# Kernel optimization log

Hardware: AMD Instinct MI355X
Metric: run time of the kernel (lower is better)

The kernel has to match this reference:

```python
import jax, jax.numpy as jnp
import numpy as np

# Hough voting constants from the call site:
# Hough(angle=90, R2_list=[4,64,256,1024], num_classes=1, region_num=13, vote_field_size=33)
ANGLE = 90
R2_LIST = (4, 64, 256, 1024)
REGION_NUM = 13
VFS = 33  # vote field size


def _hough_filter():
    """Log-polar vote-field filter [region_num, VFS, VFS].

    Region 0 = center disk (r^2 <= R2_LIST[0]); region 1 + ring*4 + angle_bin
    for the 3 radius rings x 4 angle sectors. Each region's weights are
    1/(#pixels in region) so each region's vote sums to 1 (HoughNet log map).
    """
    c = VFS // 2
    ys, xs = np.meshgrid(np.arange(VFS) - c, np.arange(VFS) - c, indexing='ij')
    r2 = xs ** 2 + ys ** 2
    theta = (np.degrees(np.arctan2(ys, xs)) + 360.0) % 360.0
    nang = 360 // ANGLE  # 4 angle sectors
    abin = np.minimum((theta // ANGLE).astype(np.int64), nang - 1)
    region = -np.ones((VFS, VFS), np.int64)
    region[r2 <= R2_LIST[0]] = 0
    for i in range(1, len(R2_LIST)):
        m = (r2 > R2_LIST[i - 1]) & (r2 <= R2_LIST[i])
        region[m] = 1 + (i - 1) * nang + abin[m]
    filt = np.zeros((REGION_NUM, VFS, VFS), np.float32)
    for r in range(REGION_NUM):
        m = region == r
        if m.sum() > 0:
            filt[r][m] = 1.0 / float(m.sum())
    return filt


# ConvTranspose2d(13 -> 1, k=33, stride=1, pad=16) == SAME conv with flipped kernel.
_HOUGH_CONV_W = jnp.asarray(np.flip(_hough_filter(), axis=(1, 2))[None].copy())  # [1,13,33,33]


def setup_inputs() -> dict:
    key = jax.random.key(0)
    ks = jax.random.split(key, 4)
    B, C, H, W = 2, 256, 256, 512
    return {
        'x': jax.random.normal(ks[0], (B, C, H, W), jnp.float32),
        'pos_w': jax.random.normal(ks[1], (13, C), jnp.float32) * 0.05,
        'pos_b': jnp.zeros((13,), jnp.float32),
        'reg_w': jax.random.normal(ks[2], (1, C), jnp.float32) * 0.05,
        'reg_b': jnp.zeros((1,), jnp.float32),
        'off_w': jax.random.normal(ks[3], (2, C), jnp.float32) * 0.05,
        'off_b': jnp.zeros((2,), jnp.float32),
    }


def _conv1x1(x, w, b):
    # x: [B,C,H,W], w: [O,C] -> [B,O,H,W]
    return jnp.einsum('bchw,oc->bohw', x, w) + b[None, :, None, None]


def reference(x, pos_w, pos_b, reg_w, reg_b, off_w, off_b):
    evident = jax.nn.relu(_conv1x1(x, pos_w, pos_b))  # [B,13,H,W]
    score = jax.lax.conv_general_dilated(
        evident, _HOUGH_CONV_W, (1, 1), 'SAME',
        dimension_numbers=('NCHW', 'OIHW', 'NCHW'))  # [B,1,H,W]
    x_cls = jax.nn.sigmoid(score)
    x_reg = _conv1x1(x, reg_w, reg_b)
    x_off = _conv1x1(x, off_w, off_b)
    return (x_cls, x_reg, x_off)
```

## Files before the change

### kernel.cpp

```cpp
#include <hip/hip_runtime.h>
#include <math.h>

#define BB   2
#define CC   256
#define HH   256
#define WW   512
#define HW   (HH*WW)
#define IMG  (CC*HW)
#define NPIX (BB*HW)

#define HP   (HH+32)
#define WP   (WW+32)
#define CHP  (HP*WP)
#define EVB  (13*CHP)
#define EV_FLOATS (BB*EVB)

#define OUT_REG (BB*HW)
#define OUT_OFF (2*BB*HW)

__global__ void repack_w(const float* __restrict__ pw, const float* __restrict__ pb,
                         const float* __restrict__ rw, const float* __restrict__ rb,
                         const float* __restrict__ ow, const float* __restrict__ ob,
                         float* __restrict__ wp, float* __restrict__ bias) {
    int i = blockIdx.x * blockDim.x + threadIdx.x;
    if (i < 4096) {
        int c = i >> 4, o = i & 15;
        float v;
        if (o < 13)       v = pw[o * CC + c];
        else if (o == 13) v = rw[c];
        else              v = ow[(o - 14) * CC + c];
        wp[c * 16 + o] = v;
    }
    if (i < 16) {
        float v = (i < 13) ? pb[i] : (i == 13 ? rb[0] : ob[i - 14]);
        bias[i] = v;
    }
}

__global__ __launch_bounds__(256) void conv1x1_k(
    const float* __restrict__ x, const float* __restrict__ wp,
    const float* __restrict__ bias, float* __restrict__ ev,
    float* __restrict__ out) {
    int g  = blockIdx.x * 256 + threadIdx.x;
    int p  = g * 2;
    int b  = p >> 17;
    int hw = p & (HW - 1);
    const float* xb = x + (size_t)b * IMG + hw;

    float acc0[16], acc1[16];
#pragma unroll
    for (int o = 0; o < 16; o++) { acc0[o] = 0.f; acc1[o] = 0.f; }

#pragma unroll 4
    for (int c = 0; c < CC; c++) {
        float2 v = *(const float2*)(xb + c * HW);
        const float* wr = wp + c * 16;
#pragma unroll
        for (int o = 0; o < 16; o++) {
            float wv = wr[o];
            acc0[o] = fmaf(v.x, wv, acc0[o]);
            acc1[o] = fmaf(v.y, wv, acc1[o]);
        }
    }

    int y0 = hw >> 9, x0 = hw & 511;
    int hw1 = hw + 1;
    int y1 = hw1 >> 9, x1 = hw1 & 511;
    float* evb = ev + (size_t)b * EVB;
#pragma unroll
    for (int o = 0; o < 13; o++) {
        float bo = bias[o];
        float e0 = fmaxf(acc0[o] + bo, 0.f);
        float e1 = fmaxf(acc1[o] + bo, 0.f);
        evb[o * CHP + (y0 + 16) * WP + (x0 + 16)] = e0;
        evb[o * CHP + (y1 + 16) * WP + (x1 + 16)] = e1;
    }
    float rbv = bias[13];
    out[OUT_REG + b * HW + hw]     = acc0[13] + rbv;
    out[OUT_REG + b * HW + hw + 1] = acc1[13] + rbv;
#pragma unroll
    for (int o = 14; o < 16; o++) {
        float bo = bias[o];
        out[OUT_OFF + b * 2 * HW + (o - 14) * HW + hw]     = acc0[o] + bo;
        out[OUT_OFF + b * 2 * HW + (o - 14) * HW + hw + 1] = acc1[o] + bo;
    }
}

__global__ __launch_bounds__(256) void hough_k(const float* __restrict__ ev,
                                               float* __restrict__ out) {
    __shared__ int   t_off[1089];
    __shared__ float t_wgt[1089];
    __shared__ int   cnt[13];
    int tid = threadIdx.x;
    if (tid < 13) cnt[tid] = 0;
    __syncthreads();

    for (int i = tid; i < 1089; i += 256) {
        int ky = i / 33, kx = i - ky * 33;
        int ys = 16 - ky, xs = 16 - kx;
        int r2 = ys * ys + xs * xs;
        int bin;
        if (ys == 0)     bin = (xs >= 0) ? 0 : 2;
        else if (ys > 0) bin = (xs > 0) ? 0 : 1;
        else             bin = (xs < 0) ? 2 : 3;
        int c;
        if (r2 <= 4)        c = 0;
        else if (r2 <= 64)  c = 1 + bin;
        else if (r2 <= 256) c = 5 + bin;
        else                c = 9 + bin;
        t_off[i] = c;
        atomicAdd(&cnt[c], 1);
    }
    __syncthreads();

    for (int i = tid; i < 1089; i += 256) {
        int ky = i / 33, kx = i - ky * 33;
        int c  = t_off[i];
        t_wgt[i] = 1.0f / (float)cnt[c];
        t_off[i] = c * CHP + (ky - 16) * WP + (kx - 16);
    }
    __syncthreads();

    int p  = blockIdx.x * 256 + tid;
    int b  = p >> 17;
    int hw = p & (HW - 1);
    int y  = hw >> 9, xx = hw & 511;
    const float* pc = ev + (size_t)b * EVB + (y + 16) * WP + (xx + 16);

    float s = 0.f;
#pragma unroll 8
    for (int t = 0; t < 1089; t++) {
        s = fmaf(pc[t_off[t]], t_wgt[t], s);
    }
    float cls = 1.0f / (1.0f + expf(-s));
    out[b * HW + hw] = cls;
}

extern "C" void kernel_launch(void* const* d_in, const int* in_sizes, int n_in,
                              void* d_out, int out_size, void* d_ws, size_t ws_size,
                              hipStream_t stream) {
    const float* x  = (const float*)d_in[0];
    const float* pw = (const float*)d_in[1];
    const float* pb = (const float*)d_in[2];
    const float* rw = (const float*)d_in[3];
    const float* rb = (const float*)d_in[4];
    const float* ow = (const float*)d_in[5];
    const float* ob = (const float*)d_in[6];
    float* out = (float*)d_out;

    float* ev   = (float*)d_ws;
    float* wp   = ev + EV_FLOATS;
    float* bias = wp + 4096;

    hipMemsetAsync(ev, 0, (size_t)EV_FLOATS * sizeof(float), stream);
    repack_w<<<16, 256, 0, stream>>>(pw, pb, rw, rb, ow, ob, wp, bias);
    conv1x1_k<<<512, 256, 0, stream>>>(x, wp, bias, ev, out);
    hough_k<<<1024, 256, 0, stream>>>(ev, out);
}
```

Before: 470.9 us.

## Store evidence maps in bf16, stage weights in LDS, pack hough table, swizzle blocks

Evidence maps are now written as bf16 (packed two per 32-bit store) instead of fp32, halving the intermediate buffer, its memset and the gather traffic in the Hough pass. The 1x1 conv stages the repacked weights in shared memory and uses vectorized float2 output stores. The Hough kernel packs offset and weight into one int2 LDS table and remaps block indices so concurrently running blocks cover different image regions. The bf16 rounding of the evidence adds precision loss to the vote sum before the sigmoid.

```diff
diff --git a/kernel.cpp b/kernel.cpp
--- a/kernel.cpp
+++ b/kernel.cpp
@@ -7,16 +7,21 @@
 #define WW   512
 #define HW   (HH*WW)
 #define IMG  (CC*HW)
-#define NPIX (BB*HW)
 
 #define HP   (HH+32)
 #define WP   (WW+32)
 #define CHP  (HP*WP)
 #define EVB  (13*CHP)
-#define EV_FLOATS (BB*EVB)
+#define EV_ELEMS (BB*EVB)
 
 #define OUT_REG (BB*HW)
 #define OUT_OFF (2*BB*HW)
+
+static __device__ __forceinline__ unsigned short f2bf_rn(float f) {
+    unsigned int u = __float_as_uint(f);
+    u += 0x7fffu + ((u >> 16) & 1u);
+    return (unsigned short)(u >> 16);
+}
 
 __global__ void repack_w(const float* __restrict__ pw, const float* __restrict__ pb,
                          const float* __restrict__ rw, const float* __restrict__ rb,
@@ -39,9 +44,16 @@
 
 __global__ __launch_bounds__(256) void conv1x1_k(
     const float* __restrict__ x, const float* __restrict__ wp,
-    const float* __restrict__ bias, float* __restrict__ ev,
+    const float* __restrict__ bias, unsigned short* __restrict__ ev,
     float* __restrict__ out) {
-    int g  = blockIdx.x * 256 + threadIdx.x;
+    __shared__ float4 wlds[1024];
+    int tid = threadIdx.x;
+    const float4* wp4 = (const float4*)wp;
+#pragma unroll
+    for (int j = 0; j < 4; j++) wlds[tid + j * 256] = wp4[tid + j * 256];
+    __syncthreads();
+
+    int g  = blockIdx.x * 256 + tid;
     int p  = g * 2;
     int b  = p >> 17;
     int hw = p & (HW - 1);
@@ -51,46 +63,47 @@
 #pragma unroll
     for (int o = 0; o < 16; o++) { acc0[o] = 0.f; acc1[o] = 0.f; }
 
-#pragma unroll 4
+#pragma unroll 2
     for (int c = 0; c < CC; c++) {
         float2 v = *(const float2*)(xb + c * HW);
-        const float* wr = wp + c * 16;
+        float4 w[4];
+#pragma unroll
+        for (int j = 0; j < 4; j++) w[j] = wlds[c * 4 + j];
+        const float* wf = (const float*)w;
 #pragma unroll
         for (int o = 0; o < 16; o++) {
-            float wv = wr[o];
+            float wv = wf[o];
             acc0[o] = fmaf(v.x, wv, acc0[o]);
             acc1[o] = fmaf(v.y, wv, acc1[o]);
         }
     }
 
     int y0 = hw >> 9, x0 = hw & 511;
-    int hw1 = hw + 1;
-    int y1 = hw1 >> 9, x1 = hw1 & 511;
-    float* evb = ev + (size_t)b * EVB;
+    unsigned short* evb = ev + (size_t)b * EVB;
+    unsigned int* evrow;
 #pragma unroll
     for (int o = 0; o < 13; o++) {
         float bo = bias[o];
         float e0 = fmaxf(acc0[o] + bo, 0.f);
         float e1 = fmaxf(acc1[o] + bo, 0.f);
-        evb[o * CHP + (y0 + 16) * WP + (x0 + 16)] = e0;
-        evb[o * CHP + (y1 + 16) * WP + (x1 + 16)] = e1;
+        unsigned int pack = (unsigned int)f2bf_rn(e0) | ((unsigned int)f2bf_rn(e1) << 16);
+        evrow = (unsigned int*)(evb + o * CHP + (y0 + 16) * WP + (x0 + 16));
+        *evrow = pack;
     }
     float rbv = bias[13];
-    out[OUT_REG + b * HW + hw]     = acc0[13] + rbv;
-    out[OUT_REG + b * HW + hw + 1] = acc1[13] + rbv;
+    *(float2*)(out + OUT_REG + b * HW + hw) = make_float2(acc0[13] + rbv, acc1[13] + rbv);
 #pragma unroll
     for (int o = 14; o < 16; o++) {
         float bo = bias[o];
-        out[OUT_OFF + b * 2 * HW + (o - 14) * HW + hw]     = acc0[o] + bo;
-        out[OUT_OFF + b * 2 * HW + (o - 14) * HW + hw + 1] = acc1[o] + bo;
+        *(float2*)(out + OUT_OFF + b * 2 * HW + (o - 14) * HW + hw) =
+            make_float2(acc0[o] + bo, acc1[o] + bo);
     }
 }
 
-__global__ __launch_bounds__(256) void hough_k(const float* __restrict__ ev,
+__global__ __launch_bounds__(256) void hough_k(const unsigned short* __restrict__ ev,
                                                float* __restrict__ out) {
-    __shared__ int   t_off[1089];
-    __shared__ float t_wgt[1089];
-    __shared__ int   cnt[13];
+    __shared__ int2 tab[1089];
+    __shared__ int  cnt[13];
     int tid = threadIdx.x;
     if (tid < 13) cnt[tid] = 0;
     __syncthreads();
@@ -108,29 +121,33 @@
         else if (r2 <= 64)  c = 1 + bin;
         else if (r2 <= 256) c = 5 + bin;
         else                c = 9 + bin;
-        t_off[i] = c;
+        tab[i].x = c;
         atomicAdd(&cnt[c], 1);
     }
     __syncthreads();
 
     for (int i = tid; i < 1089; i += 256) {
         int ky = i / 33, kx = i - ky * 33;
-        int c  = t_off[i];
-        t_wgt[i] = 1.0f / (float)cnt[c];
-        t_off[i] = c * CHP + (ky - 16) * WP + (kx - 16);
+        int c  = tab[i].x;
+        float w = 1.0f / (float)cnt[c];
+        tab[i] = make_int2(c * CHP + (ky - 16) * WP + (kx - 16), __float_as_int(w));
     }
     __syncthreads();
 
-    int p  = blockIdx.x * 256 + tid;
-    int b  = p >> 17;
-    int hw = p & (HW - 1);
-    int y  = hw >> 9, xx = hw & 511;
-    const float* pc = ev + (size_t)b * EVB + (y + 16) * WP + (xx + 16);
+    int bid = blockIdx.x;
+    int sb  = (bid & 7) * 128 + (bid >> 3);
+    int p   = sb * 256 + tid;
+    int b   = p >> 17;
+    int hw  = p & (HW - 1);
+    int y   = hw >> 9, xx = hw & 511;
+    const unsigned short* pc = ev + (size_t)b * EVB + (y + 16) * WP + (xx + 16);
 
     float s = 0.f;
 #pragma unroll 8
     for (int t = 0; t < 1089; t++) {
-        s = fmaf(pc[t_off[t]], t_wgt[t], s);
+        int2 e = tab[t];
+        float f = __uint_as_float(((unsigned int)pc[e.x]) << 16);
+        s = fmaf(f, __int_as_float(e.y), s);
     }
     float cls = 1.0f / (1.0f + expf(-s));
     out[b * HW + hw] = cls;
@@ -148,11 +165,11 @@
     const float* ob = (const float*)d_in[6];
     float* out = (float*)d_out;
 
-    float* ev   = (float*)d_ws;
-    float* wp   = ev + EV_FLOATS;
+    unsigned short* ev = (unsigned short*)d_ws;
+    float* wp   = (float*)(ev + EV_ELEMS);
     float* bias = wp + 4096;
 
-    hipMemsetAsync(ev, 0, (size_t)EV_FLOATS * sizeof(float), stream);
+    hipMemsetAsync(ev, 0, (size_t)EV_ELEMS * sizeof(unsigned short), stream);
     repack_w<<<16, 256, 0, stream>>>(pw, pb, rw, rb, ow, ob, wp, bias);
     conv1x1_k<<<512, 256, 0, stream>>>(x, wp, bias, ev, out);
     hough_k<<<1024, 256, 0, stream>>>(ev, out);
```

New measurement: 468.9 us. About the same (-0.4%).
